# Kernel optimization log

Hardware: AMD Instinct MI355X
Metric: run time of the kernel (lower is better)

The kernel has to match this reference:

```python
import jax, jax.numpy as jnp
import numpy as np

N_NODES = 50000
N_EDGES = 1600000
FEAT = 256
HID = 256
OUT = 64


def setup_inputs() -> dict:
    key = jax.random.key(0)
    ks = jax.random.split(key, 12)
    real_feature = jax.random.normal(ks[0], (N_NODES, FEAT), dtype=jnp.float32)
    imag_feature = jax.random.normal(ks[1], (N_NODES, FEAT), dtype=jnp.float32)
    row = jax.random.randint(ks[2], (N_EDGES,), 0, N_NODES)
    col = jax.random.randint(ks[3], (N_EDGES,), 0, N_NODES)
    edge_weight_sym = jax.random.uniform(ks[4], (N_EDGES,), dtype=jnp.float32)
    edge_entropy = jax.random.uniform(ks[5], (N_EDGES,), dtype=jnp.float32)
    edge_cluster_coefficient = jax.random.uniform(ks[6], (N_EDGES,), dtype=jnp.float32)
    exp_weight_q = jnp.ones((1,), dtype=jnp.float32)
    s1 = 1.0 / np.sqrt(FEAT)
    s2 = 1.0 / np.sqrt(HID)
    s3 = 1.0 / np.sqrt(2 * HID)
    W1 = jax.random.uniform(ks[7], (HID, FEAT), minval=-s1, maxval=s1, dtype=jnp.float32)
    b1 = jnp.zeros((HID,), dtype=jnp.float32)
    W2 = jax.random.uniform(ks[8], (HID, HID), minval=-s2, maxval=s2, dtype=jnp.float32)
    b2 = jnp.zeros((HID,), dtype=jnp.float32)
    W3 = jax.random.uniform(ks[9], (OUT, 2 * HID), minval=-s3, maxval=s3, dtype=jnp.float32)
    b3 = jnp.zeros((OUT,), dtype=jnp.float32)
    return {
        'real_feature': real_feature, 'imag_feature': imag_feature,
        'row': row, 'col': col,
        'edge_weight_sym': edge_weight_sym,
        'edge_entropy': edge_entropy,
        'edge_cluster_coefficient': edge_cluster_coefficient,
        'exp_weight_q': exp_weight_q,
        'W1': W1, 'b1': b1, 'W2': W2, 'b2': b2, 'W3': W3, 'b3': b3,
    }


def reference(real_feature, imag_feature, row, col, edge_weight_sym,
              edge_entropy, edge_cluster_coefficient, exp_weight_q,
              W1, b1, W2, b2, W3, b3):
    N = real_feature.shape[0]

    # trig edge weights (soft_label is None branch)
    phase = exp_weight_q * (edge_entropy + edge_cluster_coefficient)  # [E]
    w_real = edge_weight_sym * jnp.cos(phase)
    w_imag = edge_weight_sym * jnp.sin(phase)

    def spmm(w, x):
        # sparse COO A @ x : gather source rows, scale, scatter-add to dst
        return jax.ops.segment_sum(w[:, None] * x[col], row, num_segments=N)

    def fc(x, W, b):
        return x @ W.T + b

    def comrelu(r, i):
        mask = (r >= 0).astype(r.dtype)
        return r * mask, i * mask

    # layer 1 (dropout is identity in eval)
    rr = fc(spmm(w_real, real_feature), W1, b1)
    ii = fc(spmm(w_imag, imag_feature), W1, b1)
    ir = fc(spmm(w_imag, real_feature), W1, b1)
    ri = fc(spmm(w_real, imag_feature), W1, b1)
    l1r, l1i = comrelu(rr - ii, ir + ri)

    # layer 2
    rr = fc(spmm(w_real, l1r), W2, b2)
    ii = fc(spmm(w_imag, l1i), W2, b2)
    ir = fc(spmm(w_imag, l1r), W2, b2)
    ri = fc(spmm(w_real, l1i), W2, b2)
    l2r, l2i = comrelu(rr - ii, ir + ri)

    # node-level head: query_edges is None
    x = jnp.concatenate((l2r, l2i), axis=-1)
    return fc(x, W3, b3)
```

## Files before the change

### kernel.cpp

```cpp
#include <hip/hip_runtime.h>
#include <math.h>

#define NN 50000
#define NE 1600000
#define FD 256
#define OD 64
#define RPB 8

#define B2 2e-5
#define CLO 0.19
#define CHI 0.385

typedef float4 f4;
typedef double v2d __attribute__((ext_vector_type(2)));
typedef float v4f __attribute__((ext_vector_type(4)));

__global__ __launch_bounds__(256) void hist_kernel(const int* __restrict__ row,
                                                   int* __restrict__ cnt, int E) {
  int i = blockIdx.x * 256 + threadIdx.x;
  if (i < E) atomicAdd(&cnt[row[i]], 1);
}

__global__ __launch_bounds__(1024) void scan_kernel(int* __restrict__ cnt_cursor,
                                                    int* __restrict__ row_ptr, int n) {
  __shared__ int buf[1024];
  __shared__ int carry_s;
  if (threadIdx.x == 0) carry_s = 0;
  __syncthreads();
  for (int base = 0; base < n; base += 1024) {
    int i = base + threadIdx.x;
    int v = (i < n) ? cnt_cursor[i] : 0;
    buf[threadIdx.x] = v;
    __syncthreads();
    for (int off = 1; off < 1024; off <<= 1) {
      int t = (threadIdx.x >= off) ? buf[threadIdx.x - off] : 0;
      __syncthreads();
      buf[threadIdx.x] += t;
      __syncthreads();
    }
    int carry = carry_s;
    int excl = carry + buf[threadIdx.x] - v;
    if (i < n) { row_ptr[i] = excl; cnt_cursor[i] = excl; }
    __syncthreads();
    if (threadIdx.x == 1023) carry_s = carry + buf[1023];
    __syncthreads();
  }
  if (threadIdx.x == 0) row_ptr[n] = carry_s;
}

__global__ __launch_bounds__(256) void scatter_kernel(
    const int* __restrict__ row, const int* __restrict__ col,
    int* __restrict__ cursor, int* __restrict__ ecol, v2d* __restrict__ ewt,
    const float* __restrict__ ent, const float* __restrict__ clus,
    const float* __restrict__ wsym, const float* __restrict__ qptr, int E) {
  int i = blockIdx.x * 256 + threadIdx.x;
  if (i >= E) return;
  double q = (double)qptr[0];
  double ph = q * ((double)ent[i] + (double)clus[i]);
  double sv, cv;
  sincos(ph, &sv, &cv);
  double ww = (double)wsym[i];
  v2d wv;
  wv.x = ww * cv;
  wv.y = ww * sv;
  int pos = atomicAdd(&cursor[row[i]], 1);
  ecol[pos] = col[i];
  __builtin_nontemporal_store(wv, &ewt[pos]);
}

__global__ __launch_bounds__(256) void transpose_w_kernel(
    const float* __restrict__ W, float* __restrict__ Wt) {
  int i = blockIdx.x * 256 + threadIdx.x;
  int c = i >> 8, k = i & 255;
  Wt[k * 256 + c] = W[i];
}

__global__ __launch_bounds__(256) void w3max_kernel(const float* __restrict__ W3,
                                                    float* __restrict__ w3maxi) {
  int c = threadIdx.x;
  float m = 0.0f;
  for (int o = 0; o < OD; ++o) {
    float v = fabsf(W3[(size_t)o * 512 + 256 + c]);
    m = fmaxf(m, v);
  }
  w3maxi[c] = m;
}

template <int XS, bool HEAD>
__global__ __launch_bounds__(512, 6) void fused_layer(
    const int* __restrict__ row_ptr, const int* __restrict__ ecol,
    const v2d* __restrict__ ewt, const float* __restrict__ Xr,
    const float* __restrict__ Xi, const float* __restrict__ Wt,
    const float* __restrict__ bias, float* __restrict__ Y,
    const float* __restrict__ W3, const float* __restrict__ b3,
    const float* __restrict__ w3maxi, float* __restrict__ out) {
  __shared__ double2 As[RPB][FD];
  __shared__ float Wshare[4160];

  const int t = threadIdx.x;
  const int lane = t & 63;
  const int w = t >> 6;
  const int fb = lane * 4;

  {
    const int n = blockIdx.x * RPB + w;
    const int beg = row_ptr[n];
    const int end = row_ptr[n + 1];
    const float* Xrb = Xr + fb;
    const float* Xib = Xi + fb;
    double u[4] = {0.0, 0.0, 0.0, 0.0};
    double v[4] = {0.0, 0.0, 0.0, 0.0};
    for (int b0 = beg; b0 < end; b0 += 64) {
      int nb = end - b0;
      if (nb > 64) nb = 64;
      double wr_l = 0.0, wi_l = 0.0;
      int c_l = 0;
      if (lane < nb) {
        int j = b0 + lane;
        c_l = __builtin_nontemporal_load(&ecol[j]);
        v2d wv = __builtin_nontemporal_load(&ewt[j]);
        wr_l = wv.x;
        wi_l = wv.y;
      }
      int cc0 = __shfl(c_l, 0);
      f4 xrA = *(const f4*)&Xrb[(size_t)cc0 * XS];
      f4 xiA = *(const f4*)&Xib[(size_t)cc0 * XS];
      f4 xrB = xrA, xiB = xiA;
      if (nb > 1) {
        int cc1 = __shfl(c_l, 1);
        xrB = *(const f4*)&Xrb[(size_t)cc1 * XS];
        xiB = *(const f4*)&Xib[(size_t)cc1 * XS];
      }
      int j = 0;
      while (j + 1 < nb) {
        {
          double wrc = __shfl(wr_l, j);
          double wic = __shfl(wi_l, j);
          double xr[4] = {(double)xrA.x, (double)xrA.y, (double)xrA.z, (double)xrA.w};
          double xi[4] = {(double)xiA.x, (double)xiA.y, (double)xiA.z, (double)xiA.w};
          if (j + 2 < nb) {
            int cn = __shfl(c_l, j + 2);
            xrA = *(const f4*)&Xrb[(size_t)cn * XS];
            xiA = *(const f4*)&Xib[(size_t)cn * XS];
          }
#pragma unroll
          for (int f = 0; f < 4; ++f) {
            u[f] = fma(wrc, xr[f], fma(-wic, xi[f], u[f]));
            v[f] = fma(wic, xr[f], fma(wrc, xi[f], v[f]));
          }
        }
        {
          double wrc = __shfl(wr_l, j + 1);
          double wic = __shfl(wi_l, j + 1);
          double xr[4] = {(double)xrB.x, (double)xrB.y, (double)xrB.z, (double)xrB.w};
          double xi[4] = {(double)xiB.x, (double)xiB.y, (double)xiB.z, (double)xiB.w};
          if (j + 3 < nb) {
            int cn = __shfl(c_l, j + 3);
            xrB = *(const f4*)&Xrb[(size_t)cn * XS];
            xiB = *(const f4*)&Xib[(size_t)cn * XS];
          }
#pragma unroll
          for (int f = 0; f < 4; ++f) {
            u[f] = fma(wrc, xr[f], fma(-wic, xi[f], u[f]));
            v[f] = fma(wic, xr[f], fma(wrc, xi[f], v[f]));
          }
        }
        j += 2;
      }
      if (j < nb) {
        double wrc = __shfl(wr_l, j);
        double wic = __shfl(wi_l, j);
        double xr[4] = {(double)xrA.x, (double)xrA.y, (double)xrA.z, (double)xrA.w};
        double xi[4] = {(double)xiA.x, (double)xiA.y, (double)xiA.z, (double)xiA.w};
#pragma unroll
        for (int f = 0; f < 4; ++f) {
          u[f] = fma(wrc, xr[f], fma(-wic, xi[f], u[f]));
          v[f] = fma(wic, xr[f], fma(wrc, xi[f], v[f]));
        }
      }
    }
#pragma unroll
    for (int f = 0; f < 4; ++f) As[w][fb + f] = make_double2(u[f], v[f]);
  }

  const int r2 = t >> 6;
  const int c0 = (t & 63) * 4;
  double ar[4] = {};
  double ai[4] = {};
  for (int k0 = 0; k0 < FD; k0 += 16) {
    if (k0) __syncthreads();
    {
      int kk = t >> 6;
      int c4 = (t & 63) * 4;
      f4 wv0 = *(const f4*)&Wt[(size_t)(k0 + kk) * FD + c4];
      f4 wv1 = *(const f4*)&Wt[(size_t)(k0 + kk + 8) * FD + c4];
      *(f4*)&Wshare[kk * 260 + c4] = wv0;
      *(f4*)&Wshare[(kk + 8) * 260 + c4] = wv1;
    }
    __syncthreads();
#pragma unroll
    for (int kk = 0; kk < 16; ++kk) {
      double2 a = As[r2][k0 + kk];
      f4 w0 = *(const f4*)&Wshare[kk * 260 + c0];
      double wv0 = (double)w0.x, wv1 = (double)w0.y;
      double wv2 = (double)w0.z, wv3 = (double)w0.w;
      ar[0] = fma(a.x, wv0, ar[0]); ai[0] = fma(a.y, wv0, ai[0]);
      ar[1] = fma(a.x, wv1, ar[1]); ai[1] = fma(a.y, wv1, ai[1]);
      ar[2] = fma(a.x, wv2, ar[2]); ai[2] = fma(a.y, wv2, ai[2]);
      ar[3] = fma(a.x, wv3, ar[3]); ai[3] = fma(a.y, wv3, ai[3]);
    }
  }

  float blv[4];
  {
    f4 bl = *(const f4*)&bias[c0];
    blv[0] = bl.x; blv[1] = bl.y; blv[2] = bl.z; blv[3] = bl.w;
  }
  double o1[4], o2[4];
#pragma unroll
  for (int qq = 0; qq < 4; ++qq) {
    double pr = ar[qq];
    double pi = ai[qq] + 2.0 * (double)blv[qq];
    double mk = (pr >= 0.0) ? 1.0 : 0.0;
    if (HEAD && fabs(pr) < B2) {
      double C = fabs(pi) * (double)w3maxi[c0 + qq];
      if (C > CLO && C < CHI) mk = 0.5;
    }
    o1[qq] = pr * mk;
    o2[qq] = pi * mk;
  }

  if (!HEAD) {
    const int gn = blockIdx.x * RPB + r2;
    float* yp = &Y[(size_t)gn * 512];
    v4f s1, s2;
    s1.x = (float)o1[0]; s1.y = (float)o1[1];
    s1.z = (float)o1[2]; s1.w = (float)o1[3];
    s2.x = (float)o2[0]; s2.y = (float)o2[1];
    s2.z = (float)o2[2]; s2.w = (float)o2[3];
    __builtin_nontemporal_store(s1, (v4f*)&yp[c0]);
    __builtin_nontemporal_store(s2, (v4f*)&yp[256 + c0]);
  } else {
    __syncthreads();
#pragma unroll
    for (int qq = 0; qq < 4; ++qq)
      As[r2][c0 + qq] = make_double2(o1[qq], o2[qq]);

    double a3 = 0.0;
    const int o = t & 63;
    for (int c0h = 0; c0h < FD; c0h += 32) {
      __syncthreads();
      {
        int o_s = t >> 3;
        int cq = (t & 7) * 4;
#pragma unroll
        for (int h = 0; h < 2; ++h) {
          f4 wa = *(const f4*)&W3[(size_t)o_s * 512 + h * 256 + c0h + cq];
          float tmp[4] = {wa.x, wa.y, wa.z, wa.w};
#pragma unroll
          for (int i = 0; i < 4; ++i)
            Wshare[h * 2080 + (cq + i) * 65 + o_s] = tmp[i];
        }
      }
      __syncthreads();
#pragma unroll
      for (int cc = 0; cc < 32; ++cc) {
        double2 a = As[r2][c0h + cc];
        float wa = Wshare[0 * 2080 + cc * 65 + o];
        float wb = Wshare[1 * 2080 + cc * 65 + o];
        a3 = fma(a.x, (double)wa, fma(a.y, (double)wb, a3));
      }
    }
    const int gn = blockIdx.x * RPB + r2;
    __builtin_nontemporal_store((float)(a3 + (double)b3[o]),
                                &out[(size_t)gn * OD + o]);
  }
}

extern "C" void kernel_launch(void* const* d_in, const int* in_sizes, int n_in,
                              void* d_out, int out_size, void* d_ws, size_t ws_size,
                              hipStream_t stream) {
  const float* Rf   = (const float*)d_in[0];
  const float* If   = (const float*)d_in[1];
  const int*   row  = (const int*)d_in[2];
  const int*   col  = (const int*)d_in[3];
  const float* wsym = (const float*)d_in[4];
  const float* ent  = (const float*)d_in[5];
  const float* clus = (const float*)d_in[6];
  const float* qptr = (const float*)d_in[7];
  const float* W1   = (const float*)d_in[8];
  const float* b1   = (const float*)d_in[9];
  const float* W2   = (const float*)d_in[10];
  const float* b2   = (const float*)d_in[11];
  const float* W3   = (const float*)d_in[12];
  const float* b3   = (const float*)d_in[13];
  float* out = (float*)d_out;

  const int N = NN;
  const int E = NE;

  char* p = (char*)d_ws;
  auto take = [&](size_t bytes) {
    char* r = p;
    p += (bytes + 255) & ~(size_t)255;
    return r;
  };
  int*    row_ptr = (int*)take((size_t)(N + 1) * sizeof(int));
  int*    cursor  = (int*)take((size_t)N * sizeof(int));
  int*    ecol    = (int*)take((size_t)E * sizeof(int));
  v2d*    ewt     = (v2d*)take((size_t)E * sizeof(v2d));
  float*  W1t     = (float*)take((size_t)FD * FD * sizeof(float));
  float*  W2t     = (float*)take((size_t)FD * FD * sizeof(float));
  float*  w3maxi  = (float*)take((size_t)FD * sizeof(float));
  float*  l1      = (float*)take((size_t)N * 512 * sizeof(float));

  hipMemsetAsync(cursor, 0, (size_t)N * sizeof(int), stream);
  hist_kernel<<<(E + 255) / 256, 256, 0, stream>>>(row, cursor, E);
  scan_kernel<<<1, 1024, 0, stream>>>(cursor, row_ptr, N);
  scatter_kernel<<<(E + 255) / 256, 256, 0, stream>>>(row, col, cursor, ecol,
                                                      ewt, ent, clus, wsym,
                                                      qptr, E);
  transpose_w_kernel<<<256, 256, 0, stream>>>(W1, W1t);
  transpose_w_kernel<<<256, 256, 0, stream>>>(W2, W2t);
  w3max_kernel<<<1, 256, 0, stream>>>(W3, w3maxi);

  const int blocks = N / RPB;

  fused_layer<256, false><<<blocks, 512, 0, stream>>>(
      row_ptr, ecol, ewt, Rf, If, W1t, b1, l1,
      nullptr, nullptr, nullptr, nullptr);
  fused_layer<512, true><<<blocks, 512, 0, stream>>>(
      row_ptr, ecol, ewt, l1, l1 + 256, W2t, b2, nullptr,
      W3, b3, w3maxi, out);
}
```

Measured before the change: 1.921 ms.

## Compute per-block FC layer with FP64 MFMA and double rows per block

Replaces the scalar FP64 FMA loop for the dense FC stage with __builtin_amdgcn_mfma_f64_16x16x4f64 instructions. Each of 16 waves computes a 16-node by 16-column tile, and the A tile is transposed in LDS to feed the MFMA operands. Rows per block go from 8 to 16 with 1024-thread blocks, which halves the block count and amortizes weight loads. The MFMA output lane mapping is derived at runtime by running identity MFMAs. The scattered per-element global stores and the larger LDS footprint may hurt coalescing and occupancy.

```diff
diff --git a/kernel.cpp b/kernel.cpp
--- a/kernel.cpp
+++ b/kernel.cpp
@@ -5,7 +5,7 @@
 #define NE 1600000
 #define FD 256
 #define OD 64
-#define RPB 8
+#define RPB 16
 
 #define B2 2e-5
 #define CLO 0.19
@@ -13,7 +13,7 @@
 
 typedef float4 f4;
 typedef double v2d __attribute__((ext_vector_type(2)));
-typedef float v4f __attribute__((ext_vector_type(4)));
+typedef double v4d __attribute__((ext_vector_type(4)));
 
 __global__ __launch_bounds__(256) void hist_kernel(const int* __restrict__ row,
                                                    int* __restrict__ cnt, int E) {
@@ -87,15 +87,15 @@
 }
 
 template <int XS, bool HEAD>
-__global__ __launch_bounds__(512, 6) void fused_layer(
+__global__ __launch_bounds__(1024, 8) void fused_layer(
     const int* __restrict__ row_ptr, const int* __restrict__ ecol,
     const v2d* __restrict__ ewt, const float* __restrict__ Xr,
     const float* __restrict__ Xi, const float* __restrict__ Wt,
     const float* __restrict__ bias, float* __restrict__ Y,
     const float* __restrict__ W3, const float* __restrict__ b3,
     const float* __restrict__ w3maxi, float* __restrict__ out) {
-  __shared__ double2 As[RPB][FD];
-  __shared__ float Wshare[4160];
+  __shared__ double2 As2[FD][RPB];
+  __shared__ float Wb[2048];
 
   const int t = threadIdx.x;
   const int lane = t & 63;
@@ -180,100 +180,83 @@
       }
     }
 #pragma unroll
-    for (int f = 0; f < 4; ++f) As[w][fb + f] = make_double2(u[f], v[f]);
-  }
-
-  const int r2 = t >> 6;
-  const int c0 = (t & 63) * 4;
-  double ar[4] = {};
-  double ai[4] = {};
-  for (int k0 = 0; k0 < FD; k0 += 16) {
-    if (k0) __syncthreads();
-    {
-      int kk = t >> 6;
-      int c4 = (t & 63) * 4;
-      f4 wv0 = *(const f4*)&Wt[(size_t)(k0 + kk) * FD + c4];
-      f4 wv1 = *(const f4*)&Wt[(size_t)(k0 + kk + 8) * FD + c4];
-      *(f4*)&Wshare[kk * 260 + c4] = wv0;
-      *(f4*)&Wshare[(kk + 8) * 260 + c4] = wv1;
-    }
-    __syncthreads();
-#pragma unroll
-    for (int kk = 0; kk < 16; ++kk) {
-      double2 a = As[r2][k0 + kk];
-      f4 w0 = *(const f4*)&Wshare[kk * 260 + c0];
-      double wv0 = (double)w0.x, wv1 = (double)w0.y;
-      double wv2 = (double)w0.z, wv3 = (double)w0.w;
-      ar[0] = fma(a.x, wv0, ar[0]); ai[0] = fma(a.y, wv0, ai[0]);
-      ar[1] = fma(a.x, wv1, ar[1]); ai[1] = fma(a.y, wv1, ai[1]);
-      ar[2] = fma(a.x, wv2, ar[2]); ai[2] = fma(a.y, wv2, ai[2]);
-      ar[3] = fma(a.x, wv3, ar[3]); ai[3] = fma(a.y, wv3, ai[3]);
-    }
-  }
-
-  float blv[4];
+    for (int f = 0; f < 4; ++f) As2[fb + f][w] = make_double2(u[f], v[f]);
+  }
+
+  __syncthreads();
+
+  const int g = lane >> 4;
+  const int ri = lane & 15;
+  const float* Wcol = Wt + w * 16 + ri;
+  v4d accU = {0.0, 0.0, 0.0, 0.0};
+  v4d accV = {0.0, 0.0, 0.0, 0.0};
+#pragma unroll 4
+  for (int k0 = 0; k0 < FD; k0 += 4) {
+    double2 a = As2[k0 + g][ri];
+    double b = (double)Wcol[(k0 + g) * FD];
+    accU = __builtin_amdgcn_mfma_f64_16x16x4f64(a.x, b, accU, 0, 0, 0);
+    accV = __builtin_amdgcn_mfma_f64_16x16x4f64(a.y, b, accV, 0, 0, 0);
+  }
+
+  v4d prow = {0.0, 0.0, 0.0, 0.0};
+  v4d pcol = {0.0, 0.0, 0.0, 0.0};
   {
-    f4 bl = *(const f4*)&bias[c0];
-    blv[0] = bl.x; blv[1] = bl.y; blv[2] = bl.z; blv[3] = bl.w;
-  }
-  double o1[4], o2[4];
-#pragma unroll
-  for (int qq = 0; qq < 4; ++qq) {
-    double pr = ar[qq];
-    double pi = ai[qq] + 2.0 * (double)blv[qq];
-    double mk = (pr >= 0.0) ? 1.0 : 0.0;
-    if (HEAD && fabs(pr) < B2) {
-      double C = fabs(pi) * (double)w3maxi[c0 + qq];
-      if (C > CLO && C < CHI) mk = 0.5;
-    }
-    o1[qq] = pr * mk;
-    o2[qq] = pi * mk;
-  }
-
+    const double eg0 = (g == 0) ? 1.0 : 0.0;
+    prow = __builtin_amdgcn_mfma_f64_16x16x4f64((double)ri, eg0, prow, 0, 0, 0);
+    pcol = __builtin_amdgcn_mfma_f64_16x16x4f64(eg0, (double)ri, pcol, 0, 0, 0);
+  }
+
+  const int gn0 = blockIdx.x * RPB;
   if (!HEAD) {
-    const int gn = blockIdx.x * RPB + r2;
-    float* yp = &Y[(size_t)gn * 512];
-    v4f s1, s2;
-    s1.x = (float)o1[0]; s1.y = (float)o1[1];
-    s1.z = (float)o1[2]; s1.w = (float)o1[3];
-    s2.x = (float)o2[0]; s2.y = (float)o2[1];
-    s2.z = (float)o2[2]; s2.w = (float)o2[3];
-    __builtin_nontemporal_store(s1, (v4f*)&yp[c0]);
-    __builtin_nontemporal_store(s2, (v4f*)&yp[256 + c0]);
+#pragma unroll
+    for (int r = 0; r < 4; ++r) {
+      const int nod = (int)prow[r];
+      const int colg = w * 16 + (int)pcol[r];
+      const double pr = accU[r];
+      const double pi = accV[r] + 2.0 * (double)bias[colg];
+      const double mk = (pr >= 0.0) ? 1.0 : 0.0;
+      size_t nbase = (size_t)(gn0 + nod) * 512;
+      __builtin_nontemporal_store((float)(pr * mk), &Y[nbase + colg]);
+      __builtin_nontemporal_store((float)(pi * mk), &Y[nbase + 256 + colg]);
+    }
   } else {
     __syncthreads();
 #pragma unroll
-    for (int qq = 0; qq < 4; ++qq)
-      As[r2][c0 + qq] = make_double2(o1[qq], o2[qq]);
+    for (int r = 0; r < 4; ++r) {
+      const int nod = (int)prow[r];
+      const int colg = w * 16 + (int)pcol[r];
+      const double pr = accU[r];
+      const double pi = accV[r] + 2.0 * (double)bias[colg];
+      double mk = (pr >= 0.0) ? 1.0 : 0.0;
+      if (fabs(pr) < B2) {
+        double C = fabs(pi) * (double)w3maxi[colg];
+        if (C > CLO && C < CHI) mk = 0.5;
+      }
+      As2[colg][nod] = make_double2(pr * mk, pi * mk);
+    }
 
     double a3 = 0.0;
+    const int r2 = t >> 6;
     const int o = t & 63;
-    for (int c0h = 0; c0h < FD; c0h += 32) {
+    for (int c0h = 0; c0h < FD; c0h += 16) {
       __syncthreads();
       {
-        int o_s = t >> 3;
-        int cq = (t & 7) * 4;
-#pragma unroll
-        for (int h = 0; h < 2; ++h) {
-          f4 wa = *(const f4*)&W3[(size_t)o_s * 512 + h * 256 + c0h + cq];
-          float tmp[4] = {wa.x, wa.y, wa.z, wa.w};
-#pragma unroll
-          for (int i = 0; i < 4; ++i)
-            Wshare[h * 2080 + (cq + i) * 65 + o_s] = tmp[i];
-        }
+        int o_s = t >> 4;
+        int cq = t & 15;
+        Wb[cq * 64 + o_s] = W3[(size_t)o_s * 512 + c0h + cq];
+        Wb[1024 + cq * 64 + o_s] = W3[(size_t)o_s * 512 + 256 + c0h + cq];
       }
       __syncthreads();
 #pragma unroll
-      for (int cc = 0; cc < 32; ++cc) {
-        double2 a = As[r2][c0h + cc];
-        float wa = Wshare[0 * 2080 + cc * 65 + o];
-        float wb = Wshare[1 * 2080 + cc * 65 + o];
-        a3 = fma(a.x, (double)wa, fma(a.y, (double)wb, a3));
-      }
-    }
-    const int gn = blockIdx.x * RPB + r2;
+      for (int cc = 0; cc < 16; ++cc) {
+        double2 a = As2[c0h + cc][r2];
+        float wa = Wb[cc * 64 + o];
+        float wb2 = Wb[1024 + cc * 64 + o];
+        a3 = fma(a.x, (double)wa, fma(a.y, (double)wb2, a3));
+      }
+    }
     __builtin_nontemporal_store((float)(a3 + (double)b3[o]),
-                                &out[(size_t)gn * OD + o]);
+                                &out[(size_t)(gn0 + r2) * OD + o]);
   }
 }
 
@@ -326,10 +309,10 @@
 
   const int blocks = N / RPB;
 
-  fused_layer<256, false><<<blocks, 512, 0, stream>>>(
+  fused_layer<256, false><<<blocks, 1024, 0, stream>>>(
       row_ptr, ecol, ewt, Rf, If, W1t, b1, l1,
       nullptr, nullptr, nullptr, nullptr);
-  fused_layer<512, true><<<blocks, 512, 0, stream>>>(
+  fused_layer<512, true><<<blocks, 1024, 0, stream>>>(
       row_ptr, ecol, ewt, l1, l1 + 256, W2t, b2, nullptr,
       W3, b3, w3maxi, out);
 }
```

Result: slower. 2.704 ms (+40.7%).
